# Kernel tuning notes

Measured on AMD Instinct MI355X. Metric: run time of the kernel, lower is better.

## Reference

```python
import jax, jax.numpy as jnp
import numpy as np

B, L, SEQ_D, PAIR_D = 4, 512, 640, 128
C, H, NL = 128, 4, 3
DH = C // H
ED = PAIR_D + 1
KNN_K = 16
E_MAX = 131072
MIN_LOOP, MIN_PROB, HP_THRESH = 4, 0.01, 0.3


def _nussinov_pairs_np(P, min_loop=MIN_LOOP, min_prob=MIN_PROB):
    # Faithful numpy port of the torch.jit Nussinov DP (vectorized over diagonals)
    Ln = P.shape[0]
    S = np.zeros((Ln, Ln), dtype=np.float64)
    lo = np.where(P >= min_prob, np.log(P / (1.0 - P + 1e-9)), 0.0)
    for d in range(min_loop + 1, Ln):
        i = np.arange(Ln - d); j = i + d
        cand = np.maximum(np.maximum(S[i + 1, j], S[i, j - 1]), S[i + 1, j - 1] + lo[i, j])
        cand = np.maximum(cand, 0.0)  # best_bif starts at 0
        if d - min_loop - 1 > 0:
            K = np.arange(1, d - min_loop)
            bif = (S[i[:, None], i[:, None] + K[None, :]] + S[i[:, None] + K[None, :] + 1, j[:, None]]).max(1)
            cand = np.maximum(cand, bif)
        S[i, j] = cand
    pairs = []; stack = [(0, Ln - 1)]; tol = 1e-9
    while stack:
        i, j = stack.pop()
        if i >= j:
            continue
        if abs(S[i, j] - S[i + 1, j]) <= tol:
            stack.append((i + 1, j))
        elif abs(S[i, j] - S[i, j - 1]) <= tol:
            stack.append((i, j - 1))
        elif P[i, j] >= min_prob and abs(S[i, j] - (S[i + 1, j - 1] + lo[i, j])) <= tol:
            pairs.append((i, j)); stack.append((i + 1, j - 1))
        else:
            for k in range(i + 1, j):
                if abs(S[i, j] - (S[i, k] + S[k + 1, j])) <= tol:
                    stack.append((i, k)); stack.append((k + 1, j)); break
    return pairs


def _build_edges_np(coords, bppm):
    # backbone + Nussinov secondary-structure + kNN + high-prob BPPM edges (per sample)
    Ln = coords.shape[0]
    a = np.arange(Ln - 1)
    src = [np.concatenate([a, a + 1])]; dst = [np.concatenate([a + 1, a])]
    ss = _nussinov_pairs_np(bppm)
    pair_set = set((min(s, d), max(s, d)) for s, d in ss)
    if ss:
        s_ = np.array([p[0] for p in ss]); d_ = np.array([p[1] for p in ss])
        src.append(np.concatenate([s_, d_])); dst.append(np.concatenate([d_, s_]))
    dist = np.linalg.norm(coords[:, None, :] - coords[None, :, :], axis=-1)
    np.fill_diagonal(dist, np.inf)
    nn = np.argpartition(dist, KNN_K, axis=1)[:, :KNN_K]
    s_k = np.repeat(np.arange(Ln), KNN_K); d_k = nn.reshape(-1)
    src.append(np.concatenate([s_k, d_k])); dst.append(np.concatenate([d_k, s_k]))
    hp = np.triu(bppm >= HP_THRESH, 1)
    idx = np.arange(Ln - 1); hp[idx, idx + 1] = False
    for (pi, pj) in pair_set:
        hp[pi, pj] = False
    s_h, d_h = np.nonzero(hp)
    src.append(np.concatenate([s_h, d_h])); dst.append(np.concatenate([d_h, s_h]))
    return np.concatenate(src).astype(np.int64), np.concatenate(dst).astype(np.int64)


def _setup_common():
    rng = np.random.default_rng(0)
    seq = rng.standard_normal((B, L, SEQ_D)).astype(np.float32)
    pair = (rng.standard_normal((B, L, L, PAIR_D)) * 0.5).astype(np.float32)
    u = rng.random((B, L, L)) ** 40  # sparse, realistic BPPM (few high-prob pairs)
    bppm = ((u + np.swapaxes(u, 1, 2)) * 0.5).astype(np.float32)
    for b in range(B):
        np.fill_diagonal(bppm[b], 0.0)
    coords = np.cumsum(rng.standard_normal((B, L, 3)) * 2.0, axis=1).astype(np.float32)
    srcs, dsts = [], []
    for b in range(B):
        s, d = _build_edges_np(coords[b], bppm[b].astype(np.float64))
        srcs.append(s + b * L); dsts.append(d + b * L)
    src = np.concatenate(srcs)[:E_MAX]; dst = np.concatenate(dsts)[:E_MAX]
    E = src.shape[0]
    mask = np.zeros(E_MAX, dtype=np.float32); mask[:E] = 1.0
    src_p = np.zeros(E_MAX, dtype=np.int32); src_p[:E] = src
    dst_p = np.zeros(E_MAX, dtype=np.int32); dst_p[:E] = dst

    def w(*shape, scale):
        return (rng.standard_normal(shape) * scale).astype(np.float32)
    params = dict(
        W_in=w(SEQ_D, C, scale=SEQ_D ** -0.5),
        Wq=w(NL, C, C, scale=C ** -0.5), Wk=w(NL, C, C, scale=C ** -0.5),
        Wv=w(NL, C, C, scale=C ** -0.5), Wo=w(NL, C, C, scale=C ** -0.5),
        We=w(NL, ED, C, scale=ED ** -0.5), wd=w(NL, 1, C, scale=0.01),
        wx=w(NL, C, 1, scale=C ** -0.5),
        ln_g=np.ones((NL, C), dtype=np.float32), ln_b=np.zeros((NL, C), dtype=np.float32))
    inp = dict(sequence_rep=seq, pair_rep=pair, bppm=bppm, initial_coords=coords, **params,
               src=src_p, dst=dst_p, edge_mask=mask)
    return {k: jnp.asarray(v) for k, v in inp.items()}


def _seg_softmax(logits, seg, n):
    m = jax.ops.segment_max(logits, seg, num_segments=n)
    m = jnp.where(jnp.isfinite(m), m, 0.0)
    ex = jnp.exp(logits - m[seg])
    den = jax.ops.segment_sum(ex, seg, num_segments=n)
    return ex / (den[seg] + 1e-9)


def _forward(sequence_rep, pair_rep, bppm, initial_coords, W_in, Wq, Wk, Wv, Wo,
             We, wd, wx, ln_g, ln_b, edge_mask, src, dst):
    N = B * L
    h = sequence_rep.reshape(N, SEQ_D) @ W_in          # degree-0 node feats [N,C]
    x = initial_coords.reshape(N, 3)                    # degree-1 node feats [N,3]
    bidx = src // L
    i = src - bidx * L
    j = dst - bidx * L
    # per-edge features: gathered pair embedding + BPPM prob (edge fiber dim = 129)
    e = jnp.concatenate([pair_rep[bidx, i, j], bppm[bidx, i, j][:, None]], axis=-1)
    mask = edge_mask[:, None]
    for l in range(NL):
        rel = x[src] - x[dst]                           # [E,3] equivariant displacement
        d2 = jnp.sum(rel * rel, axis=-1, keepdims=True)  # [E,1] invariant
        q = (h @ Wq[l])[dst].reshape(-1, H, DH)
        k = (h @ Wk[l])[src].reshape(-1, H, DH)
        v = (h @ Wv[l])[src].reshape(-1, H, DH)
        eb = jax.nn.relu(e @ We[l] + d2 * wd[l]).reshape(-1, H, DH)  # edge bias
        logits = jnp.sum(q * (k + eb), axis=-1) / np.sqrt(DH) + (mask - 1.0) * 1e9
        alpha = _seg_softmax(logits, dst, N) * mask     # [E,H] per-destination softmax
        msg = (alpha[..., None] * v).reshape(-1, C)
        agg = jax.ops.segment_sum(msg, dst, num_segments=N)  # [N,C]
        h = h + jax.nn.relu(agg @ Wo[l])
        mu = jnp.mean(h, axis=-1, keepdims=True)
        var = jnp.var(h, axis=-1, keepdims=True)
        h = (h - mu) / jnp.sqrt(var + 1e-5) * ln_g[l] + ln_b[l]
        # equivariant coordinate update (degree-1 channel)
        s = jnp.tanh((k + eb).reshape(-1, C) @ wx[l]) * alpha.mean(-1, keepdims=True) * mask
        dx = jax.ops.segment_sum(s * rel / (jnp.sqrt(d2) + 1.0), dst, num_segments=N)
        x = x + dx
    return x.reshape(B, L, 3)


def setup_inputs() -> dict:
    return _setup_common()


def reference(sequence_rep, pair_rep, bppm, initial_coords, W_in, Wq, Wk, Wv, Wo,
              We, wd, wx, ln_g, ln_b, edge_mask, src, dst):
    return _forward(sequence_rep, pair_rep, bppm, initial_coords, W_in, Wq, Wk, Wv, Wo,
                    We, wd, wx, ln_g, ln_b, edge_mask, src, dst)
```

## Files before the change

### kernel.cpp

```cpp
#include <hip/hip_runtime.h>

#define LSEQ  512
#define NNODE 2048
#define CDIM  128
#define EMAX  131072
#define NLAY  3

typedef float f32x4 __attribute__((ext_vector_type(4)));
typedef unsigned short u16x8 __attribute__((ext_vector_type(8)));

static __device__ __forceinline__ unsigned short f2bf(float x) {
  unsigned u = __float_as_uint(x);
  unsigned r = (u + 0x7fffu + ((u >> 16) & 1u)) >> 16;
  return (unsigned short)r;
}

static __device__ __forceinline__ void mfma16(f32x4& d, f32x4 a, f32x4 b) {
  asm("v_mfma_f32_16x16x32_bf16 %0, %1, %2, %0" : "+v"(d) : "v"(a), "v"(b));
}

__global__ void k_zero(int* __restrict__ p, int n) {
  int i = blockIdx.x * blockDim.x + threadIdx.x;
  if (i < n) p[i] = 0;
}

__global__ void k_count(const int* __restrict__ dst, const float* __restrict__ msk,
                        int* __restrict__ cnt) {
  int e = blockIdx.x * 256 + threadIdx.x;
  if (msk[e] != 0.f) atomicAdd(&cnt[dst[e]], 1);
}

__global__ __launch_bounds__(256) void k_scan(const int* __restrict__ cnt,
                                              int* __restrict__ rowp) {
  __shared__ int lds[256];
  int t = threadIdx.x;
  int loc[8];
  int s = 0;
#pragma unroll
  for (int i = 0; i < 8; ++i) { loc[i] = s; s += cnt[t * 8 + i]; }
  lds[t] = s;
  __syncthreads();
  for (int off = 1; off < 256; off <<= 1) {
    int v = (t >= off) ? lds[t - off] : 0;
    __syncthreads();
    lds[t] += v;
    __syncthreads();
  }
  int base = t ? lds[t - 1] : 0;
#pragma unroll
  for (int i = 0; i < 8; ++i) rowp[t * 8 + i] = base + loc[i];
  if (t == 255) rowp[NNODE] = lds[255];
}

__global__ void k_fill(const int* __restrict__ src, const int* __restrict__ dst,
                       const float* __restrict__ msk, const int* __restrict__ rowp,
                       int* __restrict__ cur, int* __restrict__ eS,
                       int* __restrict__ eD) {
  int e = blockIdx.x * 256 + threadIdx.x;
  if (msk[e] != 0.f) {
    int n = dst[e];
    int slot = atomicAdd(&cur[n], 1);
    int p = rowp[n] + slot;
    eS[p] = src[e];
    eD[p] = n;
  }
}

__global__ __launch_bounds__(256) void k_hinq(
    const float* __restrict__ seq, const float* __restrict__ Win,
    const float* __restrict__ Wq0, const float* __restrict__ Wk0,
    const float* __restrict__ Wv0, float* __restrict__ h,
    float* __restrict__ hq, float* __restrict__ hk, float* __restrict__ hv) {
  __shared__ float sSeq[4][64];
  __shared__ __align__(16) float sW[64][128];
  __shared__ float sH[4][128];
  const int tid = threadIdx.x;
  const int c = tid & 127, g = tid >> 7;
  const int nb = blockIdx.x * 4;

  float a0 = 0.f, a1 = 0.f;
  for (int kc = 0; kc < 10; ++kc) {
    if (tid < 64) {
      int n = tid >> 4, t4 = tid & 15;
      *(float4*)&sSeq[n][t4 * 4] =
          *(const float4*)&seq[(size_t)(nb + n) * 640 + kc * 64 + t4 * 4];
    }
    const float4* wsrc = (const float4*)(Win + (size_t)kc * 64 * CDIM);
#pragma unroll
    for (int i = 0; i < 8; ++i) ((float4*)sW)[tid + i * 256] = wsrc[tid + i * 256];
    __syncthreads();
#pragma unroll 8
    for (int k = 0; k < 64; ++k) {
      float w = sW[k][c];
      a0 += sSeq[g * 2][k] * w;
      a1 += sSeq[g * 2 + 1][k] * w;
    }
    __syncthreads();
  }
  h[(size_t)(nb + g * 2) * CDIM + c] = a0;
  h[(size_t)(nb + g * 2 + 1) * CDIM + c] = a1;
  sH[g * 2][c] = a0;
  sH[g * 2 + 1][c] = a1;
  __syncthreads();

  for (int ws = 0; ws < 3; ++ws) {
    const float* W = ws == 0 ? Wq0 : (ws == 1 ? Wk0 : Wv0);
    float b0 = 0.f, b1 = 0.f;
    for (int kc = 0; kc < 2; ++kc) {
      const float4* wsrc = (const float4*)(W + (size_t)kc * 64 * CDIM);
#pragma unroll
      for (int i = 0; i < 8; ++i) ((float4*)sW)[tid + i * 256] = wsrc[tid + i * 256];
      __syncthreads();
#pragma unroll 8
      for (int k = 0; k < 64; ++k) {
        float w = sW[k][c];
        b0 += sH[g * 2][kc * 64 + k] * w;
        b1 += sH[g * 2 + 1][kc * 64 + k] * w;
      }
      __syncthreads();
    }
    float* o = ws == 0 ? hq : (ws == 1 ? hk : hv);
    o[(size_t)(nb + g * 2) * CDIM + c] = b0;
    o[(size_t)(nb + g * 2 + 1) * CDIM + c] = b1;
  }
}

__global__ __launch_bounds__(256) void k_ebf(const float* __restrict__ pair,
                                             const int* __restrict__ eS,
                                             const int* __restrict__ eD,
                                             unsigned short* __restrict__ Ebf,
                                             const float* __restrict__ We,
                                             unsigned short* __restrict__ WeT) {
  int tid = threadIdx.x;
  int pos = blockIdx.x * 16 + (tid >> 4);
  int t = tid & 15;
  int s_ = eS[pos], d_ = eD[pos];
  int j = d_ - ((s_ >> 9) << 9);
  const float* rp = pair + ((size_t)s_ * LSEQ + j) * CDIM + t * 8;
  float4 v0 = *(const float4*)rp;
  float4 v1 = *(const float4*)(rp + 4);
  u16x8 ov;
  ov[0] = f2bf(v0.x); ov[1] = f2bf(v0.y); ov[2] = f2bf(v0.z); ov[3] = f2bf(v0.w);
  ov[4] = f2bf(v1.x); ov[5] = f2bf(v1.y); ov[6] = f2bf(v1.z); ov[7] = f2bf(v1.w);
  int b = pos >> 6, m = (pos >> 4) & 3, li = pos & 15;
  int ks = t >> 2, gi = t & 3;
  size_t byte = ((size_t)((b * 16 + ks * 4 + m) * 64 + gi * 16 + li)) * 16;
  *(u16x8*)((char*)Ebf + byte) = ov;

  if (blockIdx.x < 192) {
    int idx = blockIdx.x * 256 + tid;
    int l = idx >> 14;
    int rem = idx & 16383;
    int c = rem >> 7, k = rem & 127;
    WeT[idx] = f2bf(We[(size_t)(l * 129 + k) * 128 + c]);
  }
}

__global__ __launch_bounds__(256) void k_edge_mfma(
    const unsigned short* __restrict__ Ebf, const float* __restrict__ bppm,
    const float* __restrict__ xc, const float* __restrict__ hq,
    const float* __restrict__ hk, const unsigned short* __restrict__ WeTl,
    const float* __restrict__ Wel, const float* __restrict__ wdl,
    const float* __restrict__ wxl, const int* __restrict__ eS,
    const int* __restrict__ eD, float* __restrict__ logits,
    float* __restrict__ spre) {
  __shared__ __align__(16) unsigned char sA[16384];
  __shared__ __align__(16) float sEb[64 * 128];
  __shared__ float sPart[4][64];
  __shared__ int sS[64], sD[64];
  __shared__ float sBp[64], sD2[64];

  const int tid = threadIdx.x;
  const int w = tid >> 6, l = tid & 63;
  const int li = l & 15, gi = l >> 4;
  const int p0 = blockIdx.x * 64;

  f32x4 stg[4];
  const f32x4* gE = (const f32x4*)((const char*)Ebf + (size_t)p0 * 256);
#pragma unroll
  for (int r = 0; r < 4; ++r) stg[r] = gE[r * 256 + tid];

  f32x4 bf[2][4];
#pragma unroll
  for (int nt = 0; nt < 2; ++nt) {
    int c = w * 32 + nt * 16 + li;
#pragma unroll
    for (int ks = 0; ks < 4; ++ks) {
      int k0 = ks * 32 + gi * 8;
      bf[nt][ks] = *(const f32x4*)((const char*)WeTl + (size_t)(c * 128 + k0) * 2);
    }
  }

  if (tid < 64) {
    int p = p0 + tid;
    int s_ = eS[p], d_ = eD[p];
    sS[tid] = s_; sD[tid] = d_;
    int j = d_ - ((s_ >> 9) << 9);
    float rx = xc[3 * s_ + 0] - xc[3 * d_ + 0];
    float ry = xc[3 * s_ + 1] - xc[3 * d_ + 1];
    float rz = xc[3 * s_ + 2] - xc[3 * d_ + 2];
    sD2[tid] = rx * rx + ry * ry + rz * rz;
    sBp[tid] = bppm[(size_t)s_ * LSEQ + j];
  }

  f32x4* sA4 = (f32x4*)sA;
#pragma unroll
  for (int r = 0; r < 4; ++r) sA4[r * 256 + tid] = stg[r];
  __syncthreads();

  f32x4 acc[4][2];
#pragma unroll
  for (int m = 0; m < 4; ++m)
#pragma unroll
    for (int nt = 0; nt < 2; ++nt) acc[m][nt] = (f32x4){0.f, 0.f, 0.f, 0.f};

#pragma unroll
  for (int ks = 0; ks < 4; ++ks) {
    f32x4 af[4];
#pragma unroll
    for (int m = 0; m < 4; ++m) af[m] = sA4[(ks * 4 + m) * 64 + l];
#pragma unroll
    for (int m = 0; m < 4; ++m) {
      mfma16(acc[m][0], af[m], bf[0][ks]);
      mfma16(acc[m][1], af[m], bf[1][ks]);
    }
  }

  const int c0 = w * 32 + li, c1 = c0 + 16;
  const float w128_0 = Wel[128 * 128 + c0], w128_1 = Wel[128 * 128 + c1];
  const float wd0 = wdl[c0], wd1 = wdl[c1];
#pragma unroll
  for (int m = 0; m < 4; ++m) {
#pragma unroll
    for (int r = 0; r < 4; ++r) {
      int el = m * 16 + gi * 4 + r;
      float bp = sBp[el], d2v = sD2[el];
      float eb0 = fmaxf(acc[m][0][r] + bp * w128_0 + d2v * wd0, 0.f);
      float eb1 = fmaxf(acc[m][1][r] + bp * w128_1 + d2v * wd1, 0.f);
      int swz = (el & 7) << 2;
      sEb[el * 128 + (c0 ^ swz)] = eb0;
      sEb[el * 128 + (c1 ^ swz)] = eb1;
    }
  }
  __syncthreads();

  {
    const int s_ = sS[l], d_ = sD[l];
    const int swz = (l & 7) << 2;
    const float* hkr = hk + (size_t)s_ * CDIM + w * 32;
    const float* hqr = hq + (size_t)d_ * CDIM + w * 32;
    const float* wxr = wxl + w * 32;
    float lp = 0.f, sp = 0.f;
#pragma unroll
    for (int k = 0; k < 8; ++k) {
      f32x4 ebq = *(const f32x4*)&sEb[l * 128 + ((w * 32 + k * 4) ^ swz)];
      float4 hkq = *(const float4*)(hkr + k * 4);
      float4 hqq = *(const float4*)(hqr + k * 4);
      float4 wxq = *(const float4*)(wxr + k * 4);
      float keb0 = ebq[0] + hkq.x, keb1 = ebq[1] + hkq.y;
      float keb2 = ebq[2] + hkq.z, keb3 = ebq[3] + hkq.w;
      lp += hqq.x * keb0 + hqq.y * keb1 + hqq.z * keb2 + hqq.w * keb3;
      sp += wxq.x * keb0 + wxq.y * keb1 + wxq.z * keb2 + wxq.w * keb3;
    }
    logits[(size_t)(p0 + l) * 4 + w] = lp * 0.17677669529663689f;
    sPart[w][l] = sp;
  }
  __syncthreads();
  if (tid < 64)
    spre[p0 + tid] =
        tanhf(sPart[0][tid] + sPart[1][tid] + sPart[2][tid] + sPart[3][tid]);
}

__global__ __launch_bounds__(256) void k_aggf(
    const int* __restrict__ rowp, const float4* __restrict__ lg4,
    const float* __restrict__ spre, const float* __restrict__ hvin,
    const int* __restrict__ eS, const float* __restrict__ xc,
    float* __restrict__ xn, float* __restrict__ agg) {
  const int n = blockIdx.x, tid = threadIdx.x;
  const int w = tid >> 6, lane = tid & 63;
  const int st = rowp[n], deg = rowp[n + 1] - st;

  __shared__ float sA[256][4];
  __shared__ int sSe[256];
  __shared__ float sRed[4][4];
  __shared__ __align__(16) float4 sAccF[8][32];
  __shared__ float sDx[4][3];

  float m0 = -3e38f, m1 = -3e38f, m2 = -3e38f, m3 = -3e38f;
  for (int i = tid; i < deg; i += 256) {
    float4 lg = lg4[st + i];
    m0 = fmaxf(m0, lg.x); m1 = fmaxf(m1, lg.y);
    m2 = fmaxf(m2, lg.z); m3 = fmaxf(m3, lg.w);
  }
#pragma unroll
  for (int o = 32; o; o >>= 1) {
    m0 = fmaxf(m0, __shfl_xor(m0, o)); m1 = fmaxf(m1, __shfl_xor(m1, o));
    m2 = fmaxf(m2, __shfl_xor(m2, o)); m3 = fmaxf(m3, __shfl_xor(m3, o));
  }
  if (!lane) { sRed[w][0] = m0; sRed[w][1] = m1; sRed[w][2] = m2; sRed[w][3] = m3; }
  __syncthreads();
  m0 = fmaxf(fmaxf(sRed[0][0], sRed[1][0]), fmaxf(sRed[2][0], sRed[3][0]));
  m1 = fmaxf(fmaxf(sRed[0][1], sRed[1][1]), fmaxf(sRed[2][1], sRed[3][1]));
  m2 = fmaxf(fmaxf(sRed[0][2], sRed[1][2]), fmaxf(sRed[2][2], sRed[3][2]));
  m3 = fmaxf(fmaxf(sRed[0][3], sRed[1][3]), fmaxf(sRed[2][3], sRed[3][3]));
  __syncthreads();

  float dn0 = 0.f, dn1 = 0.f, dn2 = 0.f, dn3 = 0.f;
  for (int i = tid; i < deg; i += 256) {
    float4 lg = lg4[st + i];
    dn0 += __expf(lg.x - m0); dn1 += __expf(lg.y - m1);
    dn2 += __expf(lg.z - m2); dn3 += __expf(lg.w - m3);
  }
#pragma unroll
  for (int o = 32; o; o >>= 1) {
    dn0 += __shfl_xor(dn0, o); dn1 += __shfl_xor(dn1, o);
    dn2 += __shfl_xor(dn2, o); dn3 += __shfl_xor(dn3, o);
  }
  if (!lane) { sRed[w][0] = dn0; sRed[w][1] = dn1; sRed[w][2] = dn2; sRed[w][3] = dn3; }
  __syncthreads();
  dn0 = sRed[0][0] + sRed[1][0] + sRed[2][0] + sRed[3][0];
  dn1 = sRed[0][1] + sRed[1][1] + sRed[2][1] + sRed[3][1];
  dn2 = sRed[0][2] + sRed[1][2] + sRed[2][2] + sRed[3][2];
  dn3 = sRed[0][3] + sRed[1][3] + sRed[2][3] + sRed[3][3];
  const float r0 = 1.f / (dn0 + 1e-9f), r1 = 1.f / (dn1 + 1e-9f);
  const float r2 = 1.f / (dn2 + 1e-9f), r3 = 1.f / (dn3 + 1e-9f);

  const float xnx = xc[3 * n], xny = xc[3 * n + 1], xnz = xc[3 * n + 2];
  const int ch4 = tid & 31, jg = tid >> 5, hd = ch4 >> 3;
  float4 acc4 = make_float4(0.f, 0.f, 0.f, 0.f);
  float dxx = 0.f, dxy = 0.f, dxz = 0.f;

  for (int bs = 0; bs < deg; bs += 256) {
    int cnt = min(256, deg - bs);
    __syncthreads();
    if (tid < cnt) {
      int idx = st + bs + tid;
      float4 lg = lg4[idx];
      float a0 = __expf(lg.x - m0) * r0;
      float a1 = __expf(lg.y - m1) * r1;
      float a2 = __expf(lg.z - m2) * r2;
      float a3 = __expf(lg.w - m3) * r3;
      int se = eS[idx];
      sA[tid][0] = a0; sA[tid][1] = a1; sA[tid][2] = a2; sA[tid][3] = a3;
      sSe[tid] = se;
      float rx = xc[3 * se + 0] - xnx;
      float ry = xc[3 * se + 1] - xny;
      float rz = xc[3 * se + 2] - xnz;
      float dd = rx * rx + ry * ry + rz * rz;
      float s = spre[idx] * (a0 + a1 + a2 + a3) * 0.25f;
      float inv = s / (sqrtf(dd) + 1.f);
      dxx += rx * inv; dxy += ry * inv; dxz += rz * inv;
    }
    __syncthreads();
    for (int j = jg; j < cnt; j += 8) {
      float a = sA[j][hd];
      const float4 v = *(const float4*)(hvin + (size_t)sSe[j] * CDIM + ch4 * 4);
      acc4.x += a * v.x; acc4.y += a * v.y;
      acc4.z += a * v.z; acc4.w += a * v.w;
    }
  }
  sAccF[jg][ch4] = acc4;
#pragma unroll
  for (int o = 32; o; o >>= 1) {
    dxx += __shfl_xor(dxx, o);
    dxy += __shfl_xor(dxy, o);
    dxz += __shfl_xor(dxz, o);
  }
  if (!lane) { sDx[w][0] = dxx; sDx[w][1] = dxy; sDx[w][2] = dxz; }
  __syncthreads();
  if (tid == 0) {
    xn[3 * n + 0] = xnx + sDx[0][0] + sDx[1][0] + sDx[2][0] + sDx[3][0];
    xn[3 * n + 1] = xny + sDx[0][1] + sDx[1][1] + sDx[2][1] + sDx[3][1];
    xn[3 * n + 2] = xnz + sDx[0][2] + sDx[1][2] + sDx[2][2] + sDx[3][2];
  }
  if (tid < 32) {
    float4 s = sAccF[0][tid];
#pragma unroll
    for (int g = 1; g < 8; ++g) {
      float4 v = sAccF[g][tid];
      s.x += v.x; s.y += v.y; s.z += v.z; s.w += v.w;
    }
    *(float4*)&agg[(size_t)n * CDIM + tid * 4] = s;
  }
}

__global__ __launch_bounds__(256) void k_node(
    const float* __restrict__ agg, const float* __restrict__ hin,
    const float* __restrict__ Wol, const float* __restrict__ gl,
    const float* __restrict__ bl, const float* __restrict__ Wqn,
    const float* __restrict__ Wkn, const float* __restrict__ Wvn,
    float* __restrict__ hout, float* __restrict__ hq,
    float* __restrict__ hk, float* __restrict__ hv) {
  __shared__ float sAg[4][128];
  __shared__ float sHin[4][128];
  __shared__ __align__(16) float sW[64][128];
  __shared__ float sH[4][128];
  __shared__ float sRed[4][2][2];
  const int tid = threadIdx.x;
  const int c = tid & 127, g = tid >> 7;
  const int w = tid >> 6, lane = tid & 63;
  const int nb = blockIdx.x * 4;

  {
    int i = tid & 127, half = tid >> 7;
    int n = i >> 5, t4 = i & 31;
    const float* srcb = half ? hin : agg;
    float* dstb = half ? &sHin[0][0] : &sAg[0][0];
    *(float4*)&dstb[n * 128 + t4 * 4] =
        *(const float4*)&srcb[(size_t)(nb + n) * CDIM + t4 * 4];
  }
  __syncthreads();

  float o0 = 0.f, o1 = 0.f;
  for (int kc = 0; kc < 2; ++kc) {
    const float4* wsrc = (const float4*)(Wol + (size_t)kc * 64 * CDIM);
#pragma unroll
    for (int i = 0; i < 8; ++i) ((float4*)sW)[tid + i * 256] = wsrc[tid + i * 256];
    __syncthreads();
#pragma unroll 8
    for (int k = 0; k < 64; ++k) {
      float wv = sW[k][c];
      o0 += sAg[g * 2][kc * 64 + k] * wv;
      o1 += sAg[g * 2 + 1][kc * 64 + k] * wv;
    }
    __syncthreads();
  }
  float hn0 = sHin[g * 2][c] + fmaxf(o0, 0.f);
  float hn1 = sHin[g * 2 + 1][c] + fmaxf(o1, 0.f);
  float s10 = hn0, s20 = hn0 * hn0, s11 = hn1, s21 = hn1 * hn1;
#pragma unroll
  for (int o = 32; o; o >>= 1) {
    s10 += __shfl_xor(s10, o); s20 += __shfl_xor(s20, o);
    s11 += __shfl_xor(s11, o); s21 += __shfl_xor(s21, o);
  }
  if (!lane) {
    sRed[w][0][0] = s10; sRed[w][0][1] = s20;
    sRed[w][1][0] = s11; sRed[w][1][1] = s21;
  }
  __syncthreads();
  {
    float t10 = sRed[g * 2][0][0] + sRed[g * 2 + 1][0][0];
    float t20 = sRed[g * 2][0][1] + sRed[g * 2 + 1][0][1];
    float t11 = sRed[g * 2][1][0] + sRed[g * 2 + 1][1][0];
    float t21 = sRed[g * 2][1][1] + sRed[g * 2 + 1][1][1];
    float mu0 = t10 * (1.f / 128.f), mu1 = t11 * (1.f / 128.f);
    float v0 = t20 * (1.f / 128.f) - mu0 * mu0;
    float v1 = t21 * (1.f / 128.f) - mu1 * mu1;
    float gg = gl[c], bb = bl[c];
    hn0 = (hn0 - mu0) * rsqrtf(v0 + 1e-5f) * gg + bb;
    hn1 = (hn1 - mu1) * rsqrtf(v1 + 1e-5f) * gg + bb;
  }
  hout[(size_t)(nb + g * 2) * CDIM + c] = hn0;
  hout[(size_t)(nb + g * 2 + 1) * CDIM + c] = hn1;
  sH[g * 2][c] = hn0;
  sH[g * 2 + 1][c] = hn1;
  __syncthreads();

  for (int ws = 0; ws < 3; ++ws) {
    const float* W = ws == 0 ? Wqn : (ws == 1 ? Wkn : Wvn);
    float b0 = 0.f, b1 = 0.f;
    for (int kc = 0; kc < 2; ++kc) {
      const float4* wsrc = (const float4*)(W + (size_t)kc * 64 * CDIM);
#pragma unroll
      for (int i = 0; i < 8; ++i) ((float4*)sW)[tid + i * 256] = wsrc[tid + i * 256];
      __syncthreads();
#pragma unroll 8
      for (int k = 0; k < 64; ++k) {
        float wv = sW[k][c];
        b0 += sH[g * 2][kc * 64 + k] * wv;
        b1 += sH[g * 2 + 1][kc * 64 + k] * wv;
      }
      __syncthreads();
    }
    float* o = ws == 0 ? hq : (ws == 1 ? hk : hv);
    o[(size_t)(nb + g * 2) * CDIM + c] = b0;
    o[(size_t)(nb + g * 2 + 1) * CDIM + c] = b1;
  }
}

extern "C" void kernel_launch(void* const* d_in, const int* in_sizes, int n_in,
                              void* d_out, int out_size, void* d_ws, size_t ws_size,
                              hipStream_t stream) {
  const float* seq    = (const float*)d_in[0];
  const float* pair   = (const float*)d_in[1];
  const float* bppm   = (const float*)d_in[2];
  const float* coords = (const float*)d_in[3];
  const float* Win    = (const float*)d_in[4];
  const float* Wq     = (const float*)d_in[5];
  const float* Wk     = (const float*)d_in[6];
  const float* Wv     = (const float*)d_in[7];
  const float* Wo     = (const float*)d_in[8];
  const float* We     = (const float*)d_in[9];
  const float* wd     = (const float*)d_in[10];
  const float* wx     = (const float*)d_in[11];
  const float* lng    = (const float*)d_in[12];
  const float* lnb    = (const float*)d_in[13];
  const int*   src    = (const int*)d_in[14];
  const int*   dst    = (const int*)d_in[15];
  const float* emask  = (const float*)d_in[16];
  float* out = (float*)d_out;

  size_t off = 0;
  auto take = [&](size_t bytes) {
    void* p = (char*)d_ws + off;
    off += (bytes + 255) & ~(size_t)255;
    return p;
  };
  float* hA     = (float*)take((size_t)NNODE * CDIM * 4);
  float* hB     = (float*)take((size_t)NNODE * CDIM * 4);
  float* hqA    = (float*)take((size_t)NNODE * CDIM * 4);
  float* hkA    = (float*)take((size_t)NNODE * CDIM * 4);
  float* hvA    = (float*)take((size_t)NNODE * CDIM * 4);
  float* hqB    = (float*)take((size_t)NNODE * CDIM * 4);
  float* hkB    = (float*)take((size_t)NNODE * CDIM * 4);
  float* hvB    = (float*)take((size_t)NNODE * CDIM * 4);
  float* logits = (float*)take((size_t)EMAX * 4 * 4);
  float* spre   = (float*)take((size_t)EMAX * 4);
  float* agg    = (float*)take((size_t)NNODE * CDIM * 4);
  float* x0     = (float*)take((size_t)NNODE * 3 * 4);
  float* x1     = (float*)take((size_t)NNODE * 3 * 4);
  int*   cnt    = (int*)take((size_t)NNODE * 2 * 4);
  int*   cur    = cnt + NNODE;
  int*   rowp   = (int*)take((size_t)(NNODE + 1) * 4);
  int*   eS     = (int*)take((size_t)2 * EMAX * 4);
  int*   eD     = eS + EMAX;
  unsigned short* Ebf = (unsigned short*)take((size_t)EMAX * CDIM * 2);
  unsigned short* WeT = (unsigned short*)take((size_t)NLAY * CDIM * CDIM * 2);

  k_zero<<<(NNODE * 2 + 255) / 256, 256, 0, stream>>>(cnt, NNODE * 2);
  k_zero<<<(2 * EMAX) / 256, 256, 0, stream>>>(eS, 2 * EMAX);
  k_count<<<EMAX / 256, 256, 0, stream>>>(dst, emask, cnt);
  k_scan<<<1, 256, 0, stream>>>(cnt, rowp);
  k_fill<<<EMAX / 256, 256, 0, stream>>>(src, dst, emask, rowp, cur, eS, eD);

  k_ebf<<<EMAX / 16, 256, 0, stream>>>(pair, eS, eD, Ebf, We, WeT);
  k_hinq<<<NNODE / 4, 256, 0, stream>>>(seq, Win, Wq, Wk, Wv, hA, hqA, hkA, hvA);

  const float* xc = coords;
  for (int l = 0; l < NLAY; ++l) {
    const float* hqi = (l & 1) ? hqB : hqA;
    const float* hki = (l & 1) ? hkB : hkA;
    const float* hvi = (l & 1) ? hvB : hvA;
    float* hqo = (l & 1) ? hqA : hqB;
    float* hko = (l & 1) ? hkA : hkB;
    float* hvo = (l & 1) ? hvA : hvB;
    const float* hin = (l & 1) ? hB : hA;
    float* hout = (l & 1) ? hA : hB;

    k_edge_mfma<<<EMAX / 64, 256, 0, stream>>>(
        Ebf, bppm, xc, hqi, hki, WeT + (size_t)l * CDIM * CDIM,
        We + (size_t)l * 129 * CDIM, wd + (size_t)l * CDIM,
        wx + (size_t)l * CDIM, eS, eD, logits, spre);

    float* xn = (l == NLAY - 1) ? out : (l == 0 ? x0 : x1);
    k_aggf<<<NNODE, 256, 0, stream>>>(rowp, (const float4*)logits, spre, hvi,
                                      eS, xc, xn, agg);
    if (l < NLAY - 1)
      k_node<<<NNODE / 4, 256, 0, stream>>>(
          agg, hin, Wo + (size_t)l * CDIM * CDIM, lng + (size_t)l * CDIM,
          lnb + (size_t)l * CDIM, Wq + (size_t)(l + 1) * CDIM * CDIM,
          Wk + (size_t)(l + 1) * CDIM * CDIM, Wv + (size_t)(l + 1) * CDIM * CDIM,
          hout, hqo, hko, hvo);
    xc = xn;
  }
}
```

Before: 225.5 us.

## Fuse edge-feature gather into first edge layer, merge setup kernels, cache logits in LDS

Removes the standalone k_ebf kernel. Layer 0 of k_edge_mfma now gathers pair rows, converts them to bf16 straight into shared memory, and writes the packed Ebf buffer for later layers to reuse. The WeT transpose moves into k_hinq, and the two zeroing launches merge into one over a contiguous metadata region. In k_aggf, per-node logits are cached in LDS when the degree is at most 768, avoiding repeated global reads across the three softmax passes at the cost of 12KB of extra shared memory, which may lower occupancy.

Result: no change. 223.5 us (-0.9%).

```diff
diff --git a/kernel.cpp b/kernel.cpp
--- a/kernel.cpp
+++ b/kernel.cpp
@@ -5,6 +5,7 @@
 #define CDIM  128
 #define EMAX  131072
 #define NLAY  3
+#define DCAP  768
 
 typedef float f32x4 __attribute__((ext_vector_type(4)));
 typedef unsigned short u16x8 __attribute__((ext_vector_type(8)));
@@ -70,13 +71,22 @@
     const float* __restrict__ seq, const float* __restrict__ Win,
     const float* __restrict__ Wq0, const float* __restrict__ Wk0,
     const float* __restrict__ Wv0, float* __restrict__ h,
-    float* __restrict__ hq, float* __restrict__ hk, float* __restrict__ hv) {
+    float* __restrict__ hq, float* __restrict__ hk, float* __restrict__ hv,
+    const float* __restrict__ We, unsigned short* __restrict__ WeT) {
   __shared__ float sSeq[4][64];
   __shared__ __align__(16) float sW[64][128];
   __shared__ float sH[4][128];
   const int tid = threadIdx.x;
   const int c = tid & 127, g = tid >> 7;
   const int nb = blockIdx.x * 4;
+
+  if (blockIdx.x < 192) {
+    int idx = blockIdx.x * 256 + tid;
+    int l = idx >> 14;
+    int rem = idx & 16383;
+    int cc = rem >> 7, k = rem & 127;
+    WeT[idx] = f2bf(We[(size_t)(l * 129 + k) * 128 + cc]);
+  }
 
   float a0 = 0.f, a1 = 0.f;
   for (int kc = 0; kc < 10; ++kc) {
@@ -125,37 +135,6 @@
   }
 }
 
-__global__ __launch_bounds__(256) void k_ebf(const float* __restrict__ pair,
-                                             const int* __restrict__ eS,
-                                             const int* __restrict__ eD,
-                                             unsigned short* __restrict__ Ebf,
-                                             const float* __restrict__ We,
-                                             unsigned short* __restrict__ WeT) {
-  int tid = threadIdx.x;
-  int pos = blockIdx.x * 16 + (tid >> 4);
-  int t = tid & 15;
-  int s_ = eS[pos], d_ = eD[pos];
-  int j = d_ - ((s_ >> 9) << 9);
-  const float* rp = pair + ((size_t)s_ * LSEQ + j) * CDIM + t * 8;
-  float4 v0 = *(const float4*)rp;
-  float4 v1 = *(const float4*)(rp + 4);
-  u16x8 ov;
-  ov[0] = f2bf(v0.x); ov[1] = f2bf(v0.y); ov[2] = f2bf(v0.z); ov[3] = f2bf(v0.w);
-  ov[4] = f2bf(v1.x); ov[5] = f2bf(v1.y); ov[6] = f2bf(v1.z); ov[7] = f2bf(v1.w);
-  int b = pos >> 6, m = (pos >> 4) & 3, li = pos & 15;
-  int ks = t >> 2, gi = t & 3;
-  size_t byte = ((size_t)((b * 16 + ks * 4 + m) * 64 + gi * 16 + li)) * 16;
-  *(u16x8*)((char*)Ebf + byte) = ov;
-
-  if (blockIdx.x < 192) {
-    int idx = blockIdx.x * 256 + tid;
-    int l = idx >> 14;
-    int rem = idx & 16383;
-    int c = rem >> 7, k = rem & 127;
-    WeT[idx] = f2bf(We[(size_t)(l * 129 + k) * 128 + c]);
-  }
-}
-
 __global__ __launch_bounds__(256) void k_edge_mfma(
     const unsigned short* __restrict__ Ebf, const float* __restrict__ bppm,
     const float* __restrict__ xc, const float* __restrict__ hq,
@@ -163,7 +142,8 @@
     const float* __restrict__ Wel, const float* __restrict__ wdl,
     const float* __restrict__ wxl, const int* __restrict__ eS,
     const int* __restrict__ eD, float* __restrict__ logits,
-    float* __restrict__ spre) {
+    float* __restrict__ spre, const float* __restrict__ pair,
+    unsigned short* __restrict__ EbfOut, int gather) {
   __shared__ __align__(16) unsigned char sA[16384];
   __shared__ __align__(16) float sEb[64 * 128];
   __shared__ float sPart[4][64];
@@ -176,9 +156,30 @@
   const int p0 = blockIdx.x * 64;
 
   f32x4 stg[4];
-  const f32x4* gE = (const f32x4*)((const char*)Ebf + (size_t)p0 * 256);
-#pragma unroll
-  for (int r = 0; r < 4; ++r) stg[r] = gE[r * 256 + tid];
+  if (!gather) {
+    const f32x4* gE = (const f32x4*)((const char*)Ebf + (size_t)p0 * 256);
+#pragma unroll
+    for (int r = 0; r < 4; ++r) stg[r] = gE[r * 256 + tid];
+  } else {
+#pragma unroll
+    for (int i = 0; i < 4; ++i) {
+      int slot = tid + i * 256;
+      int q = slot >> 4, t = slot & 15;
+      int p = p0 + q;
+      int s_ = eS[p], d_ = eD[p];
+      int j = d_ - ((s_ >> 9) << 9);
+      const float* rp = pair + ((size_t)s_ * LSEQ + j) * CDIM + t * 8;
+      float4 v0 = *(const float4*)rp;
+      float4 v1 = *(const float4*)(rp + 4);
+      u16x8 ov;
+      ov[0] = f2bf(v0.x); ov[1] = f2bf(v0.y); ov[2] = f2bf(v0.z); ov[3] = f2bf(v0.w);
+      ov[4] = f2bf(v1.x); ov[5] = f2bf(v1.y); ov[6] = f2bf(v1.z); ov[7] = f2bf(v1.w);
+      int m = q >> 4, lie = q & 15, ks = t >> 2, gie = t & 3;
+      int rel = ((ks * 4 + m) * 64 + gie * 16 + lie) * 16;
+      *(u16x8*)(sA + rel) = ov;
+      *(u16x8*)((char*)EbfOut + (size_t)p0 * 256 + rel) = ov;
+    }
+  }
 
   f32x4 bf[2][4];
 #pragma unroll
@@ -204,8 +205,10 @@
   }
 
   f32x4* sA4 = (f32x4*)sA;
-#pragma unroll
-  for (int r = 0; r < 4; ++r) sA4[r * 256 + tid] = stg[r];
+  if (!gather) {
+#pragma unroll
+    for (int r = 0; r < 4; ++r) sA4[r * 256 + tid] = stg[r];
+  }
   __syncthreads();
 
   f32x4 acc[4][2];
@@ -280,15 +283,19 @@
   const int w = tid >> 6, lane = tid & 63;
   const int st = rowp[n], deg = rowp[n + 1] - st;
 
+  __shared__ __align__(16) float4 sLg[DCAP];
   __shared__ float sA[256][4];
   __shared__ int sSe[256];
   __shared__ float sRed[4][4];
   __shared__ __align__(16) float4 sAccF[8][32];
   __shared__ float sDx[4][3];
 
+  const bool cached = (deg <= DCAP);
+
   float m0 = -3e38f, m1 = -3e38f, m2 = -3e38f, m3 = -3e38f;
   for (int i = tid; i < deg; i += 256) {
     float4 lg = lg4[st + i];
+    if (cached) sLg[i] = lg;
     m0 = fmaxf(m0, lg.x); m1 = fmaxf(m1, lg.y);
     m2 = fmaxf(m2, lg.z); m3 = fmaxf(m3, lg.w);
   }
@@ -307,7 +314,7 @@
 
   float dn0 = 0.f, dn1 = 0.f, dn2 = 0.f, dn3 = 0.f;
   for (int i = tid; i < deg; i += 256) {
-    float4 lg = lg4[st + i];
+    float4 lg = cached ? sLg[i] : lg4[st + i];
     dn0 += __expf(lg.x - m0); dn1 += __expf(lg.y - m1);
     dn2 += __expf(lg.z - m2); dn3 += __expf(lg.w - m3);
   }
@@ -335,7 +342,7 @@
     __syncthreads();
     if (tid < cnt) {
       int idx = st + bs + tid;
-      float4 lg = lg4[idx];
+      float4 lg = cached ? sLg[bs + tid] : lg4[idx];
       float a0 = __expf(lg.x - m0) * r0;
       float a1 = __expf(lg.y - m1) * r1;
       float a2 = __expf(lg.z - m2) * r2;
@@ -519,22 +526,23 @@
   float* agg    = (float*)take((size_t)NNODE * CDIM * 4);
   float* x0     = (float*)take((size_t)NNODE * 3 * 4);
   float* x1     = (float*)take((size_t)NNODE * 3 * 4);
-  int*   cnt    = (int*)take((size_t)NNODE * 2 * 4);
-  int*   cur    = cnt + NNODE;
+  int*   meta   = (int*)take((size_t)(NNODE * 2 + 2 * EMAX) * 4);
+  int*   cnt    = meta;
+  int*   cur    = meta + NNODE;
+  int*   eS     = meta + 2 * NNODE;
+  int*   eD     = eS + EMAX;
   int*   rowp   = (int*)take((size_t)(NNODE + 1) * 4);
-  int*   eS     = (int*)take((size_t)2 * EMAX * 4);
-  int*   eD     = eS + EMAX;
   unsigned short* Ebf = (unsigned short*)take((size_t)EMAX * CDIM * 2);
   unsigned short* WeT = (unsigned short*)take((size_t)NLAY * CDIM * CDIM * 2);
 
-  k_zero<<<(NNODE * 2 + 255) / 256, 256, 0, stream>>>(cnt, NNODE * 2);
-  k_zero<<<(2 * EMAX) / 256, 256, 0, stream>>>(eS, 2 * EMAX);
+  k_zero<<<(NNODE * 2 + 2 * EMAX + 255) / 256, 256, 0, stream>>>(
+      meta, NNODE * 2 + 2 * EMAX);
   k_count<<<EMAX / 256, 256, 0, stream>>>(dst, emask, cnt);
   k_scan<<<1, 256, 0, stream>>>(cnt, rowp);
   k_fill<<<EMAX / 256, 256, 0, stream>>>(src, dst, emask, rowp, cur, eS, eD);
 
-  k_ebf<<<EMAX / 16, 256, 0, stream>>>(pair, eS, eD, Ebf, We, WeT);
-  k_hinq<<<NNODE / 4, 256, 0, stream>>>(seq, Win, Wq, Wk, Wv, hA, hqA, hkA, hvA);
+  k_hinq<<<NNODE / 4, 256, 0, stream>>>(seq, Win, Wq, Wk, Wv, hA, hqA, hkA, hvA,
+                                        We, WeT);
 
   const float* xc = coords;
   for (int l = 0; l < NLAY; ++l) {
@@ -550,7 +558,7 @@
     k_edge_mfma<<<EMAX / 64, 256, 0, stream>>>(
         Ebf, bppm, xc, hqi, hki, WeT + (size_t)l * CDIM * CDIM,
         We + (size_t)l * 129 * CDIM, wd + (size_t)l * CDIM,
-        wx + (size_t)l * CDIM, eS, eD, logits, spre);
+        wx + (size_t)l * CDIM, eS, eD, logits, spre, pair, Ebf, l == 0 ? 1 : 0);
 
     float* xn = (l == NLAY - 1) ? out : (l == 0 ? x0 : x1);
     k_aggf<<<NNODE, 256, 0, stream>>>(rowp, (const float4*)logits, spre, hvi,
```
